# Kernel tuning notes

Hardware: AMD Instinct MI355X
Metric: run time of the kernel (lower is better)

## Reference

```python
import jax, jax.numpy as jnp
import numpy as np

B, N, IN_DIM = 4, 2048, 128
HID, OUT_DIM, HEADS = 64, 64, 4
NEG = -1e9


def setup_inputs() -> dict:
    key = jax.random.key(0)
    ks = jax.random.split(key, 6)
    x = jax.random.normal(ks[0], (B, N, IN_DIM), dtype=jnp.float32)
    adj_matrix = jax.random.randint(ks[1], (B, N, N), 0, 2, dtype=jnp.int32)
    # per-head params: W [H, IN, HID], a [H, 2*HID] (Linear(2*HID,1) weight)
    W_heads = jax.random.normal(ks[2], (HEADS, IN_DIM, HID), dtype=jnp.float32) / np.sqrt(IN_DIM)
    a_heads = jax.random.normal(ks[3], (HEADS, 2 * HID), dtype=jnp.float32) / np.sqrt(2 * HID)
    W_out = jax.random.normal(ks[4], (HEADS * HID, OUT_DIM), dtype=jnp.float32) / np.sqrt(HEADS * HID)
    a_out = jax.random.normal(ks[5], (2 * OUT_DIM,), dtype=jnp.float32) / np.sqrt(2 * OUT_DIM)
    return {"x": x, "adj_matrix": adj_matrix, "W_heads": W_heads,
            "a_heads": a_heads, "W_out": W_out, "a_out": a_out}


def gat_layer(x, W, a, adj):
    # h: [B, N, D]
    h = jnp.einsum('bni,id->bnd', x, W)
    d = h.shape[-1]
    # a . [h_i ; h_j] = h_i . a1 + h_j . a2  (avoids N^2 concat materialization)
    s = h @ a[:d]          # [B, N] source term
    t = h @ a[d:]          # [B, N] target term
    e = s[:, :, None] + t[:, None, :]              # [B, N, N]
    e = jax.nn.leaky_relu(e, negative_slope=0.2)
    e = jnp.where(adj == 0, jnp.float32(NEG), e)
    alpha = jax.nn.softmax(e, axis=-1)             # dropout is identity in eval
    return jnp.einsum('bij,bjd->bid', alpha, h)


def reference(x, adj_matrix, W_heads, a_heads, W_out, a_out):
    # multi-head: vmap over head-stacked params -> [H, B, N, HID]
    heads = jax.vmap(gat_layer, in_axes=(None, 0, 0, None))(x, W_heads, a_heads, adj_matrix)
    # concat heads along feature dim: [B, N, H*HID]
    hcat = jnp.transpose(heads, (1, 2, 0, 3)).reshape(x.shape[0], x.shape[1], -1)
    return gat_layer(hcat, W_out, a_out, adj_matrix)
```

## Files before the change

kernel.cpp:

```cpp
#include <hip/hip_runtime.h>

#define B_ 4
#define N_ 2048
#define IND_ 128
#define NH_ 4

typedef short short8 __attribute__((ext_vector_type(8)));
typedef float float4v __attribute__((ext_vector_type(4)));

#if __has_builtin(__builtin_amdgcn_sbfe)
#define SBFE(x, o) __builtin_amdgcn_sbfe((int)(x), (unsigned)(o), 1u)
#else
#define SBFE(x, o) (((int)((unsigned)(x) << (31 - (o)))) >> 31)
#endif

typedef __attribute__((address_space(1))) const unsigned int as1_u32;
typedef __attribute__((address_space(3))) unsigned int as3_u32;
__device__ __forceinline__ void gl_lds16(const void* g, void* l) {
  __builtin_amdgcn_global_load_lds((as1_u32*)g, (as3_u32*)l, 16, 0, 0);
}

__device__ __forceinline__ unsigned int f2b_bits(float f) {
  unsigned int u = __float_as_uint(f);
  u += 0x7fffu + ((u >> 16) & 1u);
  return u >> 16;
}
__device__ __forceinline__ unsigned int pack_rne(float lo, float hi) {
  return f2b_bits(lo) | (f2b_bits(hi) << 16);
}
__device__ __forceinline__ unsigned int pack_trunc(float lo, float hi) {
  return __builtin_amdgcn_perm(__float_as_uint(hi), __float_as_uint(lo), 0x07060302u);
}
__device__ __forceinline__ float trunc_bf(float f) {
  return __uint_as_float(__float_as_uint(f) & 0xFFFF0000u);
}

union u4s8 { uint4 u; short8 s; };

__global__ __launch_bounds__(256) void gat_k0(
    const int* __restrict__ adj, unsigned long long* __restrict__ adjm,
    const float* __restrict__ Wh, const float* __restrict__ ah,
    const float* __restrict__ Wo, const float* __restrict__ ao,
    uint4* __restrict__ Wpk1, uint4* __restrict__ Wpk3,
    float* __restrict__ vsp1, float* __restrict__ vsp3) {
  const int bid = blockIdx.x;
  const int t = threadIdx.x;
  if (bid < B_ * N_ * N_ / 256) {
    const int gid = bid * 256 + t;
    const unsigned long long mval = __ballot(adj[gid] != 0);
    if ((t & 63) == 0) adjm[gid >> 6] = mval;
    return;
  }
  const int pb = bid - B_ * N_ * N_ / 256;
  if (pb < 32) {
    const int id = pb * 256 + t, e = id >> 6, l = id & 63;
    const int p = e & 1, ks = (e >> 1) & 3, dt = (e >> 3) & 3, h = e >> 5;
    const int d = dt * 16 + (l & 15), kb = ks * 32 + (l >> 4) * 8;
    unsigned u[4];
#pragma unroll
    for (int i = 0; i < 4; i++) {
      float w0 = Wh[(size_t)(h * IND_ + kb + 2 * i) * 64 + d];
      float w1 = Wh[(size_t)(h * IND_ + kb + 2 * i + 1) * 64 + d];
      if (p) {
        w0 -= __uint_as_float(f2b_bits(w0) << 16);
        w1 -= __uint_as_float(f2b_bits(w1) << 16);
      }
      u[i] = pack_rne(w0, w1);
    }
    Wpk1[e * 64 + l] = make_uint4(u[0], u[1], u[2], u[3]);
  } else if (pb < 48) {
    const int id = (pb - 32) * 256 + t, e = id >> 6, l = id & 63;
    const int p = e & 1, ks = (e >> 1) & 7, dt = e >> 4;
    const int d = dt * 16 + (l & 15), kb = ks * 32 + (l >> 4) * 8;
    unsigned u[4];
#pragma unroll
    for (int i = 0; i < 4; i++) {
      float w0 = Wo[(size_t)(kb + 2 * i) * 64 + d];
      float w1 = Wo[(size_t)(kb + 2 * i + 1) * 64 + d];
      if (p) {
        w0 -= __uint_as_float(f2b_bits(w0) << 16);
        w1 -= __uint_as_float(f2b_bits(w1) << 16);
      }
      u[i] = pack_rne(w0, w1);
    }
    Wpk3[e * 64 + l] = make_uint4(u[0], u[1], u[2], u[3]);
  } else if (pb < 52) {
    const int id = (pb - 48) * 256 + t;
    const int h = id >> 8, vec = (id >> 7) & 1, k = id & 127;
    const float* wr = Wh + (size_t)(h * IND_ + k) * 64;
    const float* av = ah + h * 128 + vec * 64;
    float s = 0.f;
#pragma unroll 8
    for (int d = 0; d < 64; d++) s = fmaf(wr[d], av[d], s);
    vsp1[(h * 2 + vec) * 128 + k] = s;
  } else {
    const int id = (pb - 52) * 256 + t;
    const int vec = id >> 8, k = id & 255;
    const float* wr = Wo + (size_t)k * 64;
    const float* av = ao + vec * 64;
    float s = 0.f;
#pragma unroll 8
    for (int d = 0; d < 64; d++) s = fmaf(wr[d], av[d], s);
    vsp3[vec * 256 + k] = s;
  }
}

__global__ __launch_bounds__(256) void gat_k1(
    const float* __restrict__ x, const uint4* __restrict__ Wpk1,
    const float* __restrict__ vsp1,
    unsigned short* __restrict__ h1T, float2* __restrict__ Es1, float2* __restrict__ Et1) {
  __shared__ float xf[16 * 132];
  __shared__ unsigned short xhi[16 * 136];
  __shared__ unsigned short xlo[16 * 136];
  const int b = blockIdx.y, j0 = blockIdx.x * 16;
  const int tid = threadIdx.x;
  const int jr = tid >> 4, k0 = (tid & 15) * 8;
  const float4* xg = (const float4*)(x + ((size_t)b * N_ + j0 + jr) * IND_ + k0);
  const float4 v0 = xg[0], v1 = xg[1];
  *(float4*)(xf + jr * 132 + k0) = v0;
  *(float4*)(xf + jr * 132 + k0 + 4) = v1;
  {
    unsigned hu[4], lu[4];
    hu[0] = pack_trunc(v0.x, v0.y); hu[1] = pack_trunc(v0.z, v0.w);
    hu[2] = pack_trunc(v1.x, v1.y); hu[3] = pack_trunc(v1.z, v1.w);
    lu[0] = pack_trunc(v0.x - trunc_bf(v0.x), v0.y - trunc_bf(v0.y));
    lu[1] = pack_trunc(v0.z - trunc_bf(v0.z), v0.w - trunc_bf(v0.w));
    lu[2] = pack_trunc(v1.x - trunc_bf(v1.x), v1.y - trunc_bf(v1.y));
    lu[3] = pack_trunc(v1.z - trunc_bf(v1.z), v1.w - trunc_bf(v1.w));
    *(uint4*)(xhi + jr * 136 + k0) = make_uint4(hu[0], hu[1], hu[2], hu[3]);
    *(uint4*)(xlo + jr * 136 + k0) = make_uint4(lu[0], lu[1], lu[2], lu[3]);
  }
  __syncthreads();
  const int h = tid >> 6, lane = tid & 63;
  const int m = lane & 15, q = lane >> 4;
  float4v acc[4] = {};
  const unsigned short* ap = xhi + m * 136 + q * 8;
  const unsigned short* alp = xlo + m * 136 + q * 8;
#pragma unroll
  for (int ks = 0; ks < 4; ks++) {
    const short8 ahi = *(const short8*)(ap + ks * 32);
    const short8 alo = *(const short8*)(alp + ks * 32);
#pragma unroll
    for (int dt = 0; dt < 4; dt++) {
      u4s8 bh, bl;
      bh.u = Wpk1[(((h * 4 + dt) * 4 + ks) * 2 + 0) * 64 + lane];
      bl.u = Wpk1[(((h * 4 + dt) * 4 + ks) * 2 + 1) * 64 + lane];
      acc[dt] = __builtin_amdgcn_mfma_f32_16x16x32_bf16(ahi, bh.s, acc[dt], 0, 0, 0);
      acc[dt] = __builtin_amdgcn_mfma_f32_16x16x32_bf16(alo, bh.s, acc[dt], 0, 0, 0);
      acc[dt] = __builtin_amdgcn_mfma_f32_16x16x32_bf16(ahi, bl.s, acc[dt], 0, 0, 0);
    }
  }
  const int hb = b * NH_ + h;
#pragma unroll
  for (int dt = 0; dt < 4; dt++) {
    const uint2 uu = make_uint2(pack_rne(acc[dt][0], acc[dt][1]),
                                pack_rne(acc[dt][2], acc[dt][3]));
    *(uint2*)(h1T + (size_t)(hb * 64 + dt * 16 + m) * N_ + j0 + q * 4) = uu;
  }
  const int vec = (tid >> 5) & 1, jd = (tid >> 1) & 15, half = tid & 1;
  const float* xr = xf + jd * 132 + half * 64;
  const float* vr = vsp1 + (h * 2 + vec) * 128 + half * 64;
  float dot = 0.f;
#pragma unroll
  for (int kk = 0; kk < 64; kk += 4) {
    const float4 xa = *(const float4*)(xr + kk);
    const float4 va = *(const float4*)(vr + kk);
    dot = fmaf(xa.x, va.x, dot); dot = fmaf(xa.y, va.y, dot);
    dot = fmaf(xa.z, va.z, dot); dot = fmaf(xa.w, va.w, dot);
  }
  dot += __shfl_xor(dot, 1);
  if (half == 0) {
    const float2 ev = make_float2(__expf(dot), __expf(0.2f * dot));
    if (vec == 0) Es1[(size_t)hb * N_ + j0 + jd] = ev;
    else          Et1[(size_t)hb * N_ + j0 + jd] = ev;
  }
}

__global__ __launch_bounds__(256) void gat_k2(
    const unsigned char* __restrict__ adjm, const unsigned short* __restrict__ h1T,
    const float2* __restrict__ Es1, const float2* __restrict__ Et1,
    float* __restrict__ hcat) {
  __shared__ uint4 Ebuf[1024];
  __shared__ uint4 vbuf[2][1024];
  const int b = blockIdx.z, h = blockIdx.y, i0 = blockIdx.x * 16;
  const int tid = threadIdx.x;
  const int wv = tid >> 6, lane = tid & 63;
  const int m = lane & 15, q = lane >> 4;
  const int hb = b * NH_ + h;
  const int jb = wv * 512;
  const uint4* mp = (const uint4*)(adjm + (size_t)(b * N_ + i0 + m) * (N_ / 8) + wv * 64);
  const uint4 mk0 = mp[0], mk1 = mp[1], mk2 = mp[2], mk3 = mp[3];
  const float2 G = Es1[(size_t)hb * N_ + i0 + m];
  {
    const char* es = (const char*)(Et1 + (size_t)hb * N_ + jb);
    char* ed = (char*)Ebuf + wv * 4096;
#pragma unroll
    for (int g = 0; g < 4; g++)
      gl_lds16(es + g * 1024 + lane * 16, ed + g * 1024 + lane * 16);
  }
  const int vr = lane >> 2, vslot = lane & 3;
  const unsigned short* vs_base =
      h1T + ((size_t)hb * 64 + vr) * N_ + jb + (vslot ^ (vr & 3)) * 8;
  char* ld_base = (char*)vbuf + wv * 4096 + lane * 16;
#pragma unroll
  for (int g = 0; g < 4; g++)
    gl_lds16(vs_base + (size_t)g * 16 * N_, ld_base + g * 1024);
  float4v acc[4] = {};
  float4v accS = {};
  const short8 ONES = {0x3F80, 0x3F80, 0x3F80, 0x3F80, 0x3F80, 0x3F80, 0x3F80, 0x3F80};
#pragma unroll
  for (int it = 0; it < 16; it++) {
    if (it < 15) {
#pragma unroll
      for (int g = 0; g < 4; g++)
        gl_lds16((const char*)(vs_base + (size_t)g * 16 * N_) + (it + 1) * 64,
                 ld_base + (((it + 1) & 1) << 14) + g * 1024);
      asm volatile("s_waitcnt vmcnt(4)" ::: "memory");
    } else {
      asm volatile("s_waitcnt vmcnt(0)" ::: "memory");
    }
    const uint4 mkk = (it >> 2) == 0 ? mk0 : (it >> 2) == 1 ? mk1 : (it >> 2) == 2 ? mk2 : mk3;
    const unsigned mword =
        (it & 3) == 0 ? mkk.x : (it & 3) == 1 ? mkk.y : (it & 3) == 2 ? mkk.z : mkk.w;
    const float4* ep = (const float4*)((const char*)Ebuf + wv * 4096 + it * 256 + q * 64);
    unsigned pk[4];
#pragma unroll
    for (int p = 0; p < 4; p++) {
      const float4 e2 = ep[p];
      const float w0 = fmaxf(e2.x * G.x, e2.y * G.y);
      const float w1 = fmaxf(e2.z * G.x, e2.w * G.y);
      const int a0 = SBFE(mword, q * 8 + 2 * p);
      const int a1 = SBFE(mword, q * 8 + 2 * p + 1);
      pk[p] = pack_trunc(__uint_as_float(__float_as_uint(w0) & (unsigned)a0),
                         __uint_as_float(__float_as_uint(w1) & (unsigned)a1));
    }
    union { unsigned u[4]; short8 v; } cu;
    cu.u[0] = pk[0]; cu.u[1] = pk[1]; cu.u[2] = pk[2]; cu.u[3] = pk[3];
    const char* curv = (const char*)vbuf + ((it & 1) << 14) + wv * 4096;
#pragma unroll
    for (int dt = 0; dt < 4; dt++) {
      const int row = dt * 16 + m;
      const short8 bf = *(const short8*)(curv + row * 64 + ((q ^ (row & 3)) << 4));
      acc[dt] = __builtin_amdgcn_mfma_f32_16x16x32_bf16(cu.v, bf, acc[dt], 0, 0, 0);
    }
    accS = __builtin_amdgcn_mfma_f32_16x16x32_bf16(cu.v, ONES, accS, 0, 0, 0);
  }
  __syncthreads();
  float* red = (float*)vbuf;
  float* redS = (float*)vbuf + 4096;
#pragma unroll
  for (int dt = 0; dt < 4; dt++)
#pragma unroll
    for (int r = 0; r < 4; r++)
      red[wv * 1024 + (dt * 4 + r) * 64 + lane] = acc[dt][r];
#pragma unroll
  for (int r = 0; r < 4; r++)
    redS[wv * 256 + r * 64 + lane] = accS[r];
  __syncthreads();
  float* ob = hcat + ((size_t)(b * N_ + i0)) * 256 + h * 64 + wv * 16 + m;
#pragma unroll
  for (int r = 0; r < 4; r++) {
    float v = 0.f, S = 0.f;
#pragma unroll
    for (int w2 = 0; w2 < 4; w2++) {
      v += red[w2 * 1024 + (wv * 4 + r) * 64 + lane];
      S += redS[w2 * 256 + r * 64 + lane];
    }
    ob[(size_t)(q * 4 + r) * 256] = v / S;
  }
}

__global__ __launch_bounds__(256) void gat_k3(
    const float* __restrict__ hcat, const uint4* __restrict__ Wpk3,
    const float* __restrict__ vsp3,
    unsigned short* __restrict__ h2T, float2* __restrict__ Es2, float2* __restrict__ Et2) {
  __shared__ float xf[16 * 260];
  __shared__ unsigned short xhi[16 * 264];
  __shared__ unsigned short xlo[16 * 264];
  const int b = blockIdx.y, j0 = blockIdx.x * 16;
  const int tid = threadIdx.x;
  const int jr = tid >> 4, k0 = (tid & 15) * 16;
  const float4* xg = (const float4*)(hcat + ((size_t)b * N_ + j0 + jr) * 256 + k0);
  float4 v[4];
#pragma unroll
  for (int i = 0; i < 4; i++) v[i] = xg[i];
#pragma unroll
  for (int i = 0; i < 4; i++) *(float4*)(xf + jr * 260 + k0 + 4 * i) = v[i];
  {
    unsigned hu[8], lu[8];
#pragma unroll
    for (int i = 0; i < 4; i++) {
      hu[2 * i]     = pack_trunc(v[i].x, v[i].y);
      hu[2 * i + 1] = pack_trunc(v[i].z, v[i].w);
      lu[2 * i]     = pack_trunc(v[i].x - trunc_bf(v[i].x), v[i].y - trunc_bf(v[i].y));
      lu[2 * i + 1] = pack_trunc(v[i].z - trunc_bf(v[i].z), v[i].w - trunc_bf(v[i].w));
    }
    *(uint4*)(xhi + jr * 264 + k0)     = make_uint4(hu[0], hu[1], hu[2], hu[3]);
    *(uint4*)(xhi + jr * 264 + k0 + 8) = make_uint4(hu[4], hu[5], hu[6], hu[7]);
    *(uint4*)(xlo + jr * 264 + k0)     = make_uint4(lu[0], lu[1], lu[2], lu[3]);
    *(uint4*)(xlo + jr * 264 + k0 + 8) = make_uint4(lu[4], lu[5], lu[6], lu[7]);
  }
  __syncthreads();
  const int w = tid >> 6, lane = tid & 63;
  const int m = lane & 15, q = lane >> 4;
  float4v acc = {};
  const unsigned short* ap = xhi + m * 264 + q * 8;
  const unsigned short* alp = xlo + m * 264 + q * 8;
#pragma unroll
  for (int ks = 0; ks < 8; ks++) {
    const short8 ahi = *(const short8*)(ap + ks * 32);
    const short8 alo = *(const short8*)(alp + ks * 32);
    u4s8 bh, bl;
    bh.u = Wpk3[((w * 8 + ks) * 2 + 0) * 64 + lane];
    bl.u = Wpk3[((w * 8 + ks) * 2 + 1) * 64 + lane];
    acc = __builtin_amdgcn_mfma_f32_16x16x32_bf16(ahi, bh.s, acc, 0, 0, 0);
    acc = __builtin_amdgcn_mfma_f32_16x16x32_bf16(alo, bh.s, acc, 0, 0, 0);
    acc = __builtin_amdgcn_mfma_f32_16x16x32_bf16(ahi, bl.s, acc, 0, 0, 0);
  }
  {
    const uint2 uu = make_uint2(pack_rne(acc[0], acc[1]), pack_rne(acc[2], acc[3]));
    *(uint2*)(h2T + (size_t)(b * 64 + w * 16 + m) * N_ + j0 + q * 4) = uu;
  }
  const int vec = tid >> 7, jj = (tid >> 3) & 15, seg = tid & 7;
  const float* xr = xf + jj * 260 + seg * 4;
  const float* vr = vsp3 + vec * 256 + seg * 4;
  float dot = 0.f;
#pragma unroll
  for (int s = 0; s < 8; s++) {
    const float4 xa = *(const float4*)(xr + s * 32);
    const float4 va = *(const float4*)(vr + s * 32);
    dot = fmaf(xa.x, va.x, dot); dot = fmaf(xa.y, va.y, dot);
    dot = fmaf(xa.z, va.z, dot); dot = fmaf(xa.w, va.w, dot);
  }
  dot += __shfl_xor(dot, 1);
  dot += __shfl_xor(dot, 2);
  dot += __shfl_xor(dot, 4);
  if (seg == 0) {
    const float2 ev = make_float2(__expf(dot), __expf(0.2f * dot));
    if (vec == 0) Es2[(size_t)b * N_ + j0 + jj] = ev;
    else          Et2[(size_t)b * N_ + j0 + jj] = ev;
  }
}

__global__ __launch_bounds__(256) void gat_k4(
    const unsigned char* __restrict__ adjm, const unsigned short* __restrict__ h2T,
    const float2* __restrict__ Es2, const float2* __restrict__ Et2,
    float* __restrict__ out) {
  __shared__ uint4 Ebuf[1024];
  __shared__ uint4 vbuf[2][1024];
  const int b = blockIdx.y, i0 = blockIdx.x * 16;
  const int tid = threadIdx.x;
  const int wv = tid >> 6, lane = tid & 63;
  const int m = lane & 15, q = lane >> 4;
  const int jb = wv * 512;
  const uint4* mp = (const uint4*)(adjm + (size_t)(b * N_ + i0 + m) * (N_ / 8) + wv * 64);
  const uint4 mk0 = mp[0], mk1 = mp[1], mk2 = mp[2], mk3 = mp[3];
  const float2 G = Es2[(size_t)b * N_ + i0 + m];
  {
    const char* es = (const char*)(Et2 + (size_t)b * N_ + jb);
    char* ed = (char*)Ebuf + wv * 4096;
#pragma unroll
    for (int g = 0; g < 4; g++)
      gl_lds16(es + g * 1024 + lane * 16, ed + g * 1024 + lane * 16);
  }
  const int vr = lane >> 2, vslot = lane & 3;
  const unsigned short* vs_base =
      h2T + ((size_t)b * 64 + vr) * N_ + jb + (vslot ^ (vr & 3)) * 8;
  char* ld_base = (char*)vbuf + wv * 4096 + lane * 16;
#pragma unroll
  for (int g = 0; g < 4; g++)
    gl_lds16(vs_base + (size_t)g * 16 * N_, ld_base + g * 1024);
  float4v acc[4] = {};
  float4v accS = {};
  const short8 ONES = {0x3F80, 0x3F80, 0x3F80, 0x3F80, 0x3F80, 0x3F80, 0x3F80, 0x3F80};
#pragma unroll
  for (int it = 0; it < 16; it++) {
    if (it < 15) {
#pragma unroll
      for (int g = 0; g < 4; g++)
        gl_lds16((const char*)(vs_base + (size_t)g * 16 * N_) + (it + 1) * 64,
                 ld_base + (((it + 1) & 1) << 14) + g * 1024);
      asm volatile("s_waitcnt vmcnt(4)" ::: "memory");
    } else {
      asm volatile("s_waitcnt vmcnt(0)" ::: "memory");
    }
    const uint4 mkk = (it >> 2) == 0 ? mk0 : (it >> 2) == 1 ? mk1 : (it >> 2) == 2 ? mk2 : mk3;
    const unsigned mword =
        (it & 3) == 0 ? mkk.x : (it & 3) == 1 ? mkk.y : (it & 3) == 2 ? mkk.z : mkk.w;
    const float4* ep = (const float4*)((const char*)Ebuf + wv * 4096 + it * 256 + q * 64);
    unsigned pk[4];
#pragma unroll
    for (int p = 0; p < 4; p++) {
      const float4 e2 = ep[p];
      const float w0 = fmaxf(e2.x * G.x, e2.y * G.y);
      const float w1 = fmaxf(e2.z * G.x, e2.w * G.y);
      const int a0 = SBFE(mword, q * 8 + 2 * p);
      const int a1 = SBFE(mword, q * 8 + 2 * p + 1);
      pk[p] = pack_trunc(__uint_as_float(__float_as_uint(w0) & (unsigned)a0),
                         __uint_as_float(__float_as_uint(w1) & (unsigned)a1));
    }
    union { unsigned u[4]; short8 v; } cu;
    cu.u[0] = pk[0]; cu.u[1] = pk[1]; cu.u[2] = pk[2]; cu.u[3] = pk[3];
    const char* curv = (const char*)vbuf + ((it & 1) << 14) + wv * 4096;
#pragma unroll
    for (int dt = 0; dt < 4; dt++) {
      const int row = dt * 16 + m;
      const short8 bf = *(const short8*)(curv + row * 64 + ((q ^ (row & 3)) << 4));
      acc[dt] = __builtin_amdgcn_mfma_f32_16x16x32_bf16(cu.v, bf, acc[dt], 0, 0, 0);
    }
    accS = __builtin_amdgcn_mfma_f32_16x16x32_bf16(cu.v, ONES, accS, 0, 0, 0);
  }
  __syncthreads();
  float* red = (float*)vbuf;
  float* redS = (float*)vbuf + 4096;
#pragma unroll
  for (int dt = 0; dt < 4; dt++)
#pragma unroll
    for (int r = 0; r < 4; r++)
      red[wv * 1024 + (dt * 4 + r) * 64 + lane] = acc[dt][r];
#pragma unroll
  for (int r = 0; r < 4; r++)
    redS[wv * 256 + r * 64 + lane] = accS[r];
  __syncthreads();
  float* ob = out + ((size_t)(b * N_ + i0)) * 64 + wv * 16 + m;
#pragma unroll
  for (int r = 0; r < 4; r++) {
    float v = 0.f, S = 0.f;
#pragma unroll
    for (int w2 = 0; w2 < 4; w2++) {
      v += red[w2 * 1024 + (wv * 4 + r) * 64 + lane];
      S += redS[w2 * 256 + r * 64 + lane];
    }
    ob[(size_t)(q * 4 + r) * 64] = v / S;
  }
}

extern "C" void kernel_launch(void* const* d_in, const int* in_sizes, int n_in,
                              void* d_out, int out_size, void* d_ws, size_t ws_size,
                              hipStream_t stream) {
  (void)in_sizes; (void)n_in; (void)out_size; (void)ws_size;
  const float* x  = (const float*)d_in[0];
  const int* adj  = (const int*)d_in[1];
  const float* Wh = (const float*)d_in[2];
  const float* ah = (const float*)d_in[3];
  const float* Wo = (const float*)d_in[4];
  const float* ao = (const float*)d_in[5];
  float* out = (float*)d_out;

  char* base = (char*)d_ws;
  unsigned long long* adjm = (unsigned long long*)base;
  unsigned short* h1T = (unsigned short*)(base + 0x200000);
  float2* Et1 = (float2*)(base + 0x600000);
  float2* Es1 = (float2*)(base + 0x640000);
  unsigned short* h2T = (unsigned short*)(base + 0x680000);
  float2* Et2 = (float2*)(base + 0x780000);
  float2* Es2 = (float2*)(base + 0x790000);
  uint4* Wpk1 = (uint4*)(base + 0x7A0000);
  uint4* Wpk3 = (uint4*)(base + 0x7C0000);
  float* vsp1 = (float*)(base + 0x7D0000);
  float* vsp3 = (float*)(base + 0x7D1000);
  float* hcat = (float*)(base + 0x800000);

  gat_k0<<<dim3(B_ * N_ * N_ / 256 + 54), 256, 0, stream>>>(
      adj, adjm, Wh, ah, Wo, ao, Wpk1, Wpk3, vsp1, vsp3);
  gat_k1<<<dim3(N_ / 16, B_), 256, 0, stream>>>(x, Wpk1, vsp1, h1T, Es1, Et1);
  gat_k2<<<dim3(N_ / 16, NH_, B_), 256, 0, stream>>>(
      (const unsigned char*)adjm, h1T, Es1, Et1, hcat);
  gat_k3<<<dim3(N_ / 16, B_), 256, 0, stream>>>(hcat, Wpk3, vsp3, h2T, Es2, Et2);
  gat_k4<<<dim3(N_ / 16, B_), 256, 0, stream>>>(
      (const unsigned char*)adjm, h2T, Es2, Et2, out);
}
```

Measured before the change: 183.1 us.

## Restructure head aggregation so each wave owns rows and shares value tiles

The first-layer aggregation kernel now gives each of the four waves its own 16 destination rows and has every wave sweep all source columns. One shared double-buffered value tile is reused by all waves, and the whole Et row is loaded once. This removes the cross-wave split-K reduction through LDS and cuts the grid to a quarter as many blocks, each loading values once instead of four times. The price is a block barrier on every one of 64 iterations, less parallelism, and dropping the XOR swizzle on value loads in both aggregation kernels, which may bring LDS bank conflicts.

```diff
diff --git a/kernel.cpp b/kernel.cpp
--- a/kernel.cpp
+++ b/kernel.cpp
@@ -181,48 +181,40 @@
     const float2* __restrict__ Es1, const float2* __restrict__ Et1,
     float* __restrict__ hcat) {
   __shared__ uint4 Ebuf[1024];
-  __shared__ uint4 vbuf[2][1024];
-  const int b = blockIdx.z, h = blockIdx.y, i0 = blockIdx.x * 16;
+  __shared__ uint4 vbuf[2][256];
+  const int b = blockIdx.z, h = blockIdx.y;
   const int tid = threadIdx.x;
   const int wv = tid >> 6, lane = tid & 63;
   const int m = lane & 15, q = lane >> 4;
+  const int i0 = blockIdx.x * 64 + wv * 16;
   const int hb = b * NH_ + h;
-  const int jb = wv * 512;
-  const uint4* mp = (const uint4*)(adjm + (size_t)(b * N_ + i0 + m) * (N_ / 8) + wv * 64);
-  const uint4 mk0 = mp[0], mk1 = mp[1], mk2 = mp[2], mk3 = mp[3];
+  {
+    const char* es = (const char*)(Et1 + (size_t)hb * N_);
+#pragma unroll
+    for (int c = 0; c < 4; c++)
+      gl_lds16(es + c * 4096 + tid * 16, (char*)Ebuf + c * 4096 + tid * 16);
+  }
+  const unsigned short* vsrc =
+      h1T + ((size_t)hb * 64 + (tid >> 6) * 16 + (tid & 15)) * N_ + ((tid >> 4) & 3) * 8;
+  gl_lds16(vsrc, (char*)vbuf[0] + tid * 16);
   const float2 G = Es1[(size_t)hb * N_ + i0 + m];
-  {
-    const char* es = (const char*)(Et1 + (size_t)hb * N_ + jb);
-    char* ed = (char*)Ebuf + wv * 4096;
-#pragma unroll
-    for (int g = 0; g < 4; g++)
-      gl_lds16(es + g * 1024 + lane * 16, ed + g * 1024 + lane * 16);
-  }
-  const int vr = lane >> 2, vslot = lane & 3;
-  const unsigned short* vs_base =
-      h1T + ((size_t)hb * 64 + vr) * N_ + jb + (vslot ^ (vr & 3)) * 8;
-  char* ld_base = (char*)vbuf + wv * 4096 + lane * 16;
-#pragma unroll
-  for (int g = 0; g < 4; g++)
-    gl_lds16(vs_base + (size_t)g * 16 * N_, ld_base + g * 1024);
+  const uint4* mp = (const uint4*)(adjm + (size_t)(b * N_ + i0 + m) * (N_ / 8));
+  uint4 mw_cur = mp[0];
+  uint4 mw_nxt = mp[1];
   float4v acc[4] = {};
   float4v accS = {};
   const short8 ONES = {0x3F80, 0x3F80, 0x3F80, 0x3F80, 0x3F80, 0x3F80, 0x3F80, 0x3F80};
-#pragma unroll
-  for (int it = 0; it < 16; it++) {
-    if (it < 15) {
-#pragma unroll
-      for (int g = 0; g < 4; g++)
-        gl_lds16((const char*)(vs_base + (size_t)g * 16 * N_) + (it + 1) * 64,
-                 ld_base + (((it + 1) & 1) << 14) + g * 1024);
-      asm volatile("s_waitcnt vmcnt(4)" ::: "memory");
-    } else {
-      asm volatile("s_waitcnt vmcnt(0)" ::: "memory");
-    }
-    const uint4 mkk = (it >> 2) == 0 ? mk0 : (it >> 2) == 1 ? mk1 : (it >> 2) == 2 ? mk2 : mk3;
-    const unsigned mword =
-        (it & 3) == 0 ? mkk.x : (it & 3) == 1 ? mkk.y : (it & 3) == 2 ? mkk.z : mkk.w;
-    const float4* ep = (const float4*)((const char*)Ebuf + wv * 4096 + it * 256 + q * 64);
+  for (int it = 0; it < 64; it++) {
+    __syncthreads();
+    if (it + 1 < 64)
+      gl_lds16((const char*)vsrc + (it + 1) * 64, (char*)vbuf[(it + 1) & 1] + tid * 16);
+    const int s = it & 3;
+    const unsigned mword = s == 0 ? mw_cur.x : s == 1 ? mw_cur.y : s == 2 ? mw_cur.z : mw_cur.w;
+    if (s == 3) {
+      mw_cur = mw_nxt;
+      if (it + 5 < 64) mw_nxt = mp[(it >> 2) + 2];
+    }
+    const float4* ep = (const float4*)((const char*)Ebuf + it * 256 + q * 64);
     unsigned pk[4];
 #pragma unroll
     for (int p = 0; p < 4; p++) {
@@ -236,37 +228,23 @@
     }
     union { unsigned u[4]; short8 v; } cu;
     cu.u[0] = pk[0]; cu.u[1] = pk[1]; cu.u[2] = pk[2]; cu.u[3] = pk[3];
-    const char* curv = (const char*)vbuf + ((it & 1) << 14) + wv * 4096;
+    const char* curv = (const char*)vbuf[it & 1];
 #pragma unroll
     for (int dt = 0; dt < 4; dt++) {
-      const int row = dt * 16 + m;
-      const short8 bf = *(const short8*)(curv + row * 64 + ((q ^ (row & 3)) << 4));
+      const short8 bf = *(const short8*)(curv + dt * 1024 + lane * 16);
       acc[dt] = __builtin_amdgcn_mfma_f32_16x16x32_bf16(cu.v, bf, acc[dt], 0, 0, 0);
     }
     accS = __builtin_amdgcn_mfma_f32_16x16x32_bf16(cu.v, ONES, accS, 0, 0, 0);
   }
-  __syncthreads();
-  float* red = (float*)vbuf;
-  float* redS = (float*)vbuf + 4096;
-#pragma unroll
-  for (int dt = 0; dt < 4; dt++)
-#pragma unroll
-    for (int r = 0; r < 4; r++)
-      red[wv * 1024 + (dt * 4 + r) * 64 + lane] = acc[dt][r];
-#pragma unroll
-  for (int r = 0; r < 4; r++)
-    redS[wv * 256 + r * 64 + lane] = accS[r];
-  __syncthreads();
-  float* ob = hcat + ((size_t)(b * N_ + i0)) * 256 + h * 64 + wv * 16 + m;
+  float* ob = hcat + (size_t)b * N_ * 256 + h * 64 + m;
 #pragma unroll
   for (int r = 0; r < 4; r++) {
-    float v = 0.f, S = 0.f;
-#pragma unroll
-    for (int w2 = 0; w2 < 4; w2++) {
-      v += red[w2 * 1024 + (wv * 4 + r) * 64 + lane];
-      S += redS[w2 * 256 + r * 64 + lane];
-    }
-    ob[(size_t)(q * 4 + r) * 256] = v / S;
+    const float invS = 1.0f / accS[r];
+    float* op = ob + (size_t)(i0 + q * 4 + r) * 256;
+    op[0]  = acc[0][r] * invS;
+    op[16] = acc[1][r] * invS;
+    op[32] = acc[2][r] * invS;
+    op[48] = acc[3][r] * invS;
   }
 }
 
@@ -363,13 +341,11 @@
     for (int g = 0; g < 4; g++)
       gl_lds16(es + g * 1024 + lane * 16, ed + g * 1024 + lane * 16);
   }
-  const int vr = lane >> 2, vslot = lane & 3;
-  const unsigned short* vs_base =
-      h2T + ((size_t)b * 64 + vr) * N_ + jb + (vslot ^ (vr & 3)) * 8;
+  const unsigned short* vs_row = h2T + ((size_t)b * 64 + (lane & 15)) * N_ + jb + q * 8;
   char* ld_base = (char*)vbuf + wv * 4096 + lane * 16;
 #pragma unroll
   for (int g = 0; g < 4; g++)
-    gl_lds16(vs_base + (size_t)g * 16 * N_, ld_base + g * 1024);
+    gl_lds16(vs_row + (size_t)g * 16 * N_, ld_base + g * 1024);
   float4v acc[4] = {};
   float4v accS = {};
   const short8 ONES = {0x3F80, 0x3F80, 0x3F80, 0x3F80, 0x3F80, 0x3F80, 0x3F80, 0x3F80};
@@ -378,7 +354,7 @@
     if (it < 15) {
 #pragma unroll
       for (int g = 0; g < 4; g++)
-        gl_lds16((const char*)(vs_base + (size_t)g * 16 * N_) + (it + 1) * 64,
+        gl_lds16((const char*)(vs_row + (size_t)g * 16 * N_) + (it + 1) * 64,
                  ld_base + (((it + 1) & 1) << 14) + g * 1024);
       asm volatile("s_waitcnt vmcnt(4)" ::: "memory");
     } else {
@@ -404,8 +380,7 @@
     const char* curv = (const char*)vbuf + ((it & 1) << 14) + wv * 4096;
 #pragma unroll
     for (int dt = 0; dt < 4; dt++) {
-      const int row = dt * 16 + m;
-      const short8 bf = *(const short8*)(curv + row * 64 + ((q ^ (row & 3)) << 4));
+      const short8 bf = *(const short8*)(curv + dt * 1024 + lane * 16);
       acc[dt] = __builtin_amdgcn_mfma_f32_16x16x32_bf16(cu.v, bf, acc[dt], 0, 0, 0);
     }
     accS = __builtin_amdgcn_mfma_f32_16x16x32_bf16(cu.v, ONES, accS, 0, 0, 0);
@@ -464,7 +439,7 @@
   gat_k0<<<dim3(B_ * N_ * N_ / 256 + 54), 256, 0, stream>>>(
       adj, adjm, Wh, ah, Wo, ao, Wpk1, Wpk3, vsp1, vsp3);
   gat_k1<<<dim3(N_ / 16, B_), 256, 0, stream>>>(x, Wpk1, vsp1, h1T, Es1, Et1);
-  gat_k2<<<dim3(N_ / 16, NH_, B_), 256, 0, stream>>>(
+  gat_k2<<<dim3(N_ / 64, NH_, B_), 256, 0, stream>>>(
       (const unsigned char*)adjm, h1T, Es1, Et1, hcat);
   gat_k3<<<dim3(N_ / 16, B_), 256, 0, stream>>>(hcat, Wpk3, vsp3, h2T, Es2, Et2);
   gat_k4<<<dim3(N_ / 16, B_), 256, 0, stream>>>(
```

After: 184.4 us. No clear change (+0.7%).
